# Performance work log

Measured on AMD Instinct MI355X. Metric: run time of the kernel, lower is better.

The kernel has to match this reference:

```python
import jax, jax.numpy as jnp
import numpy as np

N = 10000          # nodes
E = 160000         # random edges (self-loops added in reference, as PyG does)
HEADS = 32
DIMS = [4, 128, 512, 1028]
NEG_SLOPE_ATT = 0.2    # GATv2Conv default negative_slope
NEG_SLOPE_ACT = 0.01   # torch.nn.LeakyReLU default


def setup_inputs() -> dict:
    key = jax.random.key(0)
    ks = jax.random.split(key, 32)
    inp = {}
    inp["x"] = jax.random.normal(ks[0], (N, DIMS[0]), dtype=jnp.float32)
    inp["edge_index"] = jax.random.randint(ks[1], (2, E), 0, N, dtype=jnp.int32)
    k = 2
    for l in range(3):
        fi, fo = DIMS[l], DIMS[l + 1]
        s_in = 1.0 / np.sqrt(fi)
        s_att = 1.0 / np.sqrt(fo)
        inp[f"W{l+1}l"] = (jax.random.normal(ks[k], (fi, HEADS * fo)) * s_in).astype(jnp.float32); k += 1
        inp[f"b{l+1}l"] = jnp.zeros((HEADS * fo,), jnp.float32)
        inp[f"W{l+1}r"] = (jax.random.normal(ks[k], (fi, HEADS * fo)) * s_in).astype(jnp.float32); k += 1
        inp[f"b{l+1}r"] = jnp.zeros((HEADS * fo,), jnp.float32)
        inp[f"att{l+1}"] = (jax.random.normal(ks[k], (HEADS, fo)) * s_att).astype(jnp.float32); k += 1
        inp[f"bias{l+1}"] = jnp.zeros((fo,), jnp.float32)
    return inp


def gatv2_layer(x, src, dst, Wl, bl, Wr, br, att, bias):
    # x: [N, fi]; src/dst: [E'] (self-loops included); att: [H, C]
    H, C = att.shape
    n = x.shape[0]
    xl = (x @ Wl + bl).reshape(n, H, C)  # source transform
    xr = (x @ Wr + br).reshape(n, H, C)  # target transform

    def per_head(args):
        xlh, xrh, ah = args  # [N,C], [N,C], [C]
        s = jax.nn.leaky_relu(xlh[src] + xrh[dst], NEG_SLOPE_ATT)  # [E',C]
        e = s @ ah  # [E'] attention logits
        m = jax.ops.segment_max(e, dst, num_segments=n)
        p = jnp.exp(e - m[dst])
        den = jax.ops.segment_sum(p, dst, num_segments=n)
        alpha = p / den[dst]  # edge-softmax per destination
        return jax.ops.segment_sum(alpha[:, None] * xlh[src], dst, num_segments=n)  # [N,C]

    # iterate heads sequentially to keep peak memory at O(E*C), not O(E*H*C)
    out = jax.lax.map(per_head, (jnp.moveaxis(xl, 1, 0), jnp.moveaxis(xr, 1, 0), att))  # [H,N,C]
    return out.mean(axis=0) + bias  # concat=False -> head mean


def reference(x, edge_index, W1l, b1l, W1r, b1r, att1, bias1,
              W2l, b2l, W2r, b2r, att2, bias2,
              W3l, b3l, W3r, b3r, att3, bias3):
    n = x.shape[0]
    loop = jnp.arange(n, dtype=edge_index.dtype)
    src = jnp.concatenate([edge_index[0], loop])
    dst = jnp.concatenate([edge_index[1], loop])
    h = gatv2_layer(x, src, dst, W1l, b1l, W1r, b1r, att1, bias1)
    h = jax.nn.leaky_relu(h, NEG_SLOPE_ACT)
    h = gatv2_layer(h, src, dst, W2l, b2l, W2r, b2r, att2, bias2)
    h = jax.nn.leaky_relu(h, NEG_SLOPE_ACT)
    h = gatv2_layer(h, src, dst, W3l, b3l, W3r, b3r, att3, bias3)
    return h
```

## Files before the change

kernel.cpp:

```cpp
#include <hip/hip_runtime.h>
#include <cstddef>
#include <cstdint>


#define HEADS 32
#define SLOPE_ATT 0.2f
#define SLOPE_ACT 0.01f

typedef __bf16 bf16_t;
typedef __bf16 bf16x8 __attribute__((ext_vector_type(8)));
typedef float f32x16 __attribute__((ext_vector_type(16)));

#define GLDS16(gp, lp)                                                        \
  __builtin_amdgcn_global_load_lds(                                           \
      (const __attribute__((address_space(1))) void*)(gp),                    \
      (__attribute__((address_space(3))) void*)(lp), 16, 0, 0)


__global__ __launch_bounds__(256) void init_counts_kernel(int* counts, int n) {
  int i = blockIdx.x * 256 + threadIdx.x;
  if (i < n) counts[i] = 1;
}

__global__ __launch_bounds__(256) void count_kernel(const int* __restrict__ dst, int* counts, int E) {
  int e = blockIdx.x * 256 + threadIdx.x;
  if (e < E) atomicAdd(&counts[dst[e]], 1);
}

__global__ __launch_bounds__(1024) void scan_kernel(const int* __restrict__ counts,
                                                    int* __restrict__ row_ptr,
                                                    int* __restrict__ cursor, int n) {
  __shared__ int sums[1024];
  int t = threadIdx.x;
  int per = (n + 1023) >> 10;
  int base = t * per;
  int s = 0;
  for (int i = 0; i < per; i++) { int idx = base + i; if (idx < n) s += counts[idx]; }
  sums[t] = s;
  __syncthreads();
  for (int off = 1; off < 1024; off <<= 1) {
    int v = (t >= off) ? sums[t - off] : 0;
    __syncthreads();
    sums[t] += v;
    __syncthreads();
  }
  int run = (t == 0) ? 0 : sums[t - 1];
  for (int i = 0; i < per; i++) {
    int idx = base + i;
    if (idx < n) { row_ptr[idx] = run; cursor[idx] = run; run += counts[idx]; }
  }
  if (t == 1023) row_ptr[n] = sums[1023];
}

__global__ __launch_bounds__(256) void scatter_edges_kernel(const int* __restrict__ ei, int* cursor,
                                                            int* col_src, int* col_dst, int E) {
  int e = blockIdx.x * 256 + threadIdx.x;
  if (e >= E) return;
  int src = ei[e], dst = ei[E + e];
  int pos = atomicAdd(&cursor[dst], 1);
  col_src[pos] = src;
  col_dst[pos] = dst;
}

__global__ __launch_bounds__(256) void scatter_loops_kernel(int* cursor, int* col_src, int* col_dst, int N) {
  int nid = blockIdx.x * 256 + threadIdx.x;
  if (nid >= N) return;
  int pos = atomicAdd(&cursor[nid], 1);
  col_src[pos] = nid;
  col_dst[pos] = nid;
}


__global__ __launch_bounds__(256) void cvt_pack_kernel(const float* __restrict__ X,
                                                       bf16_t* __restrict__ hi,
                                                       bf16_t* __restrict__ lo,
                                                       int M, int Mpad, int K) {
  int t = blockIdx.x * 256 + threadIdx.x;
  int kchunks = K >> 3;
  int total = Mpad * kchunks;
  if (t >= total) return;
  int kc = t % kchunks;
  int m = t / kchunks;
  int mt = m >> 7, ml = m & 127;
  size_t o = ((size_t)(mt * kchunks + kc)) * 1024 + (size_t)ml * 8;
  float v[8];
  if (m < M) {
    float4 a = *(const float4*)(X + (size_t)m * K + kc * 8);
    float4 b = *(const float4*)(X + (size_t)m * K + kc * 8 + 4);
    v[0] = a.x; v[1] = a.y; v[2] = a.z; v[3] = a.w;
    v[4] = b.x; v[5] = b.y; v[6] = b.z; v[7] = b.w;
  } else {
#pragma unroll
    for (int i = 0; i < 8; i++) v[i] = 0.f;
  }
  union { bf16_t h[8]; float4 f; } uh, ul;
#pragma unroll
  for (int i = 0; i < 8; i++) {
    bf16_t h = (bf16_t)v[i];
    uh.h[i] = h;
    ul.h[i] = (bf16_t)(v[i] - (float)h);
  }
  *(float4*)(hi + o) = uh.f;
  *(float4*)(lo + o) = ul.f;
}


__global__ __launch_bounds__(256) void pack_w_group_kernel(const float* __restrict__ Wl,
                                                           const float* __restrict__ Wr,
                                                           bf16_t* __restrict__ hL, bf16_t* __restrict__ lL,
                                                           bf16_t* __restrict__ hR, bf16_t* __restrict__ lR,
                                                           int K, int C, int Npad, int ldW,
                                                           int h0, int G) {
  int side = blockIdx.y;
  const float* W = side ? Wr : Wl;
  bf16_t* Hi = side ? hR : hL;
  bf16_t* Lo = side ? lR : lL;
  int kchunks = K >> 3;
  int perhead = Npad * kchunks;
  int t = blockIdx.x * 256 + threadIdx.x;
  if (t >= G * perhead) return;
  int g = t / perhead, rem = t % perhead;
  int n = rem % Npad, kc = rem / Npad;
  int nt = n >> 7, nl = n & 127;
  size_t o = (size_t)g * Npad * K + ((size_t)(nt * kchunks + kc)) * 1024 + (size_t)nl * 8;
  int col0 = (h0 + g) * C;
  union { bf16_t hh[8]; float4 f; } uh, ul;
#pragma unroll
  for (int kk = 0; kk < 8; kk++) {
    int k = kc * 8 + kk;
    float v = (n < C) ? W[(size_t)k * ldW + col0 + n] : 0.f;
    bf16_t hv = (bf16_t)v;
    uh.hh[kk] = hv;
    ul.hh[kk] = (bf16_t)(v - (float)hv);
  }
  *(float4*)(Hi + o) = uh.f;
  *(float4*)(Lo + o) = ul.f;
}


__global__ __launch_bounds__(256) void gemm_mfma_v6(const bf16_t* __restrict__ Xh,
                                                    const bf16_t* __restrict__ Xl,
                                                    const bf16_t* __restrict__ BhL,
                                                    const bf16_t* __restrict__ BlL,
                                                    const bf16_t* __restrict__ BhR,
                                                    const bf16_t* __restrict__ BlR,
                                                    size_t bHeadStride,
                                                    const float* __restrict__ bl,
                                                    const float* __restrict__ br,
                                                    float* __restrict__ outL,
                                                    float* __restrict__ outR,
                                                    size_t outHeadStride,
                                                    int M, int K, int C, int h0) {
  int g = blockIdx.z >> 1, side = blockIdx.z & 1;
  const bf16_t* Bh = (side ? BhR : BhL) + (size_t)g * bHeadStride;
  const bf16_t* Bl = (side ? BlR : BlL) + (size_t)g * bHeadStride;
  const float* bias = side ? br : bl;
  float* out = (side ? outR : outL) + (size_t)g * outHeadStride;
  int col0 = (h0 + g) * C;

  __shared__ __align__(16) bf16_t AsH[4 * 128 * 8];
  __shared__ __align__(16) bf16_t AsL[4 * 128 * 8];
  __shared__ __align__(16) bf16_t BsH[4 * 128 * 8];
  __shared__ __align__(16) bf16_t BsL[4 * 128 * 8];

  int tid = threadIdx.x;
  int wave = tid >> 6, lane = tid & 63;
  int l31 = lane & 31, lhalf = lane >> 5;
  int mt = blockIdx.y;
  int ntb = blockIdx.x * 128;
  int m0 = mt * 128;
  int kchunks = K >> 3;

  const bf16_t* Ah = Xh + (size_t)mt * K * 128;
  const bf16_t* Al = Xl + (size_t)mt * K * 128;
  const bf16_t* Bhp = Bh + (size_t)blockIdx.x * kchunks * 1024;
  const bf16_t* Blp = Bl + (size_t)blockIdx.x * kchunks * 1024;

  auto* asH3 = (__attribute__((address_space(3))) bf16_t*)AsH;
  auto* asL3 = (__attribute__((address_space(3))) bf16_t*)AsL;
  auto* bsH3 = (__attribute__((address_space(3))) bf16_t*)BsH;
  auto* bsL3 = (__attribute__((address_space(3))) bf16_t*)BsL;

  f32x16 acc[4];
#pragma unroll
  for (int i = 0; i < 4; i++)
#pragma unroll
    for (int r = 0; r < 16; r++) acc[i][r] = 0.f;

  for (int k0 = 0; k0 < K; k0 += 32) {
    int kc0 = k0 >> 3;
#pragma unroll
    for (int r = 0; r < 2; r++) {
      int idx = tid + 256 * r;
      size_t off = ((size_t)(kc0 + (idx >> 7))) * 1024 + (size_t)(idx & 127) * 8;
      int li = idx * 8;
      GLDS16(Ah + off, asH3 + li);
      GLDS16(Al + off, asL3 + li);
      GLDS16(Bhp + off, bsH3 + li);
      GLDS16(Blp + off, bsL3 + li);
    }
    __syncthreads();

#pragma unroll
    for (int s = 0; s < 2; s++) {
      int c = s * 2 + lhalf;
      int abase = (c * 128 + wave * 32 + l31) * 8;
      bf16x8 ah = *(const bf16x8*)&AsH[abase];
      bf16x8 al = *(const bf16x8*)&AsL[abase];
#pragma unroll
      for (int nt = 0; nt < 4; nt++) {
        int bbase = (c * 128 + nt * 32 + l31) * 8;
        bf16x8 bh = *(const bf16x8*)&BsH[bbase];
        bf16x8 blo = *(const bf16x8*)&BsL[bbase];
        acc[nt] = __builtin_amdgcn_mfma_f32_32x32x16_bf16(ah, bh, acc[nt], 0, 0, 0);
        acc[nt] = __builtin_amdgcn_mfma_f32_32x32x16_bf16(ah, blo, acc[nt], 0, 0, 0);
        acc[nt] = __builtin_amdgcn_mfma_f32_32x32x16_bf16(al, bh, acc[nt], 0, 0, 0);
      }
    }
    __syncthreads();
  }

#pragma unroll
  for (int nt = 0; nt < 4; nt++) {
    int n = ntb + nt * 32 + l31;
    if (n >= C) continue;
    float bv = bias[col0 + n];
#pragma unroll
    for (int r = 0; r < 16; r++) {
      int row = (r & 3) + 8 * (r >> 2) + 4 * lhalf;
      int m = m0 + wave * 32 + row;
      if (m < M) out[(size_t)m * C + n] = acc[nt][r] + bv;
    }
  }
}


#define BM 128
#define BN 128
#define BK 16
#define LDA (BM + 4)
#define LDB (BN + 4)

__global__ __launch_bounds__(256) void gemm128(const float* __restrict__ X,
                                               const float* __restrict__ Wl,
                                               const float* __restrict__ Wr,
                                               const float* __restrict__ bl,
                                               const float* __restrict__ br,
                                               float* __restrict__ outL,
                                               float* __restrict__ outR,
                                               int M, int K, int C, int ldW, int col0) {
  const float* W = blockIdx.z ? Wr : Wl;
  const float* bias = blockIdx.z ? br : bl;
  float* out = blockIdx.z ? outR : outL;

  __shared__ __align__(16) float As[BK][LDA];
  __shared__ __align__(16) float Bs[BK][LDB];

  int t = threadIdx.x;
  int tx = t & 15, ty = t >> 4;
  int m0 = blockIdx.y * BM, n0 = blockIdx.x * BN;

  float acc00[4][4] = {}, acc01[4][4] = {}, acc10[4][4] = {}, acc11[4][4] = {};

  for (int k0 = 0; k0 < K; k0 += BK) {
    {
      int kk = (t & 3) * 4;
#pragma unroll
      for (int p = 0; p < 2; p++) {
        int row = (t >> 2) + p * 64;
        int m = m0 + row;
        float4 v = make_float4(0.f, 0.f, 0.f, 0.f);
        if (m < M && (k0 + kk) < K)
          v = *(const float4*)(X + (size_t)m * K + k0 + kk);
        As[kk + 0][row] = v.x; As[kk + 1][row] = v.y;
        As[kk + 2][row] = v.z; As[kk + 3][row] = v.w;
      }
    }
    {
      int kk = t >> 4;
#pragma unroll
      for (int q = 0; q < 2; q++) {
        int cn = (t & 15) * 4 + q * 64;
        int n = n0 + cn;
        float4 v = make_float4(0.f, 0.f, 0.f, 0.f);
        if ((k0 + kk) < K && n + 3 < C)
          v = *(const float4*)(W + (size_t)(k0 + kk) * ldW + col0 + n);
        *(float4*)&Bs[kk][cn] = v;
      }
    }
    __syncthreads();

    int kmax = min(BK, K - k0);
    for (int kk = 0; kk < kmax; kk++) {
      float4 a0 = *(const float4*)&As[kk][ty * 4];
      float4 a1 = *(const float4*)&As[kk][64 + ty * 4];
      float4 b0 = *(const float4*)&Bs[kk][tx * 4];
      float4 b1 = *(const float4*)&Bs[kk][64 + tx * 4];
      float af0[4] = {a0.x, a0.y, a0.z, a0.w};
      float af1[4] = {a1.x, a1.y, a1.z, a1.w};
      float bf0[4] = {b0.x, b0.y, b0.z, b0.w};
      float bf1[4] = {b1.x, b1.y, b1.z, b1.w};
#pragma unroll
      for (int i = 0; i < 4; i++)
#pragma unroll
        for (int j = 0; j < 4; j++) {
          acc00[i][j] += af0[i] * bf0[j];
          acc01[i][j] += af0[i] * bf1[j];
          acc10[i][j] += af1[i] * bf0[j];
          acc11[i][j] += af1[i] * bf1[j];
        }
    }
    __syncthreads();
  }

#pragma unroll
  for (int ma = 0; ma < 2; ma++) {
#pragma unroll
    for (int i = 0; i < 4; i++) {
      int m = m0 + ma * 64 + ty * 4 + i;
      if (m >= M) continue;
#pragma unroll
      for (int nb = 0; nb < 2; nb++) {
        int n = n0 + nb * 64 + tx * 4;
        float (*blk)[4] = (ma == 0) ? ((nb == 0) ? acc00 : acc01)
                                    : ((nb == 0) ? acc10 : acc11);
        if (n + 3 < C) {
          float4 bv = *(const float4*)(bias + col0 + n);
          float4 o = make_float4(blk[i][0] + bv.x, blk[i][1] + bv.y,
                                 blk[i][2] + bv.z, blk[i][3] + bv.w);
          *(float4*)(out + (size_t)m * C + n) = o;
        }
      }
    }
  }
}


template <int F4PT>
__global__ __launch_bounds__(256) void edge_fused_kernel(const int* __restrict__ row_ptr,
                                                         const int* __restrict__ col_src,
                                                         const float* __restrict__ xl,
                                                         const float* __restrict__ xr,
                                                         int ld4, int coff4,
                                                         const float* __restrict__ att,
                                                         float* __restrict__ acc,
                                                         int C, int head) {
  int node = blockIdx.x;
  int tid = threadIdx.x;
  int wave = tid >> 6, lane = tid & 63;
  int C4 = C >> 2;
  int s = row_ptr[node], t = row_ptr[node + 1];

  __shared__ __align__(16) float4 slab[4][F4PT * 64];
  __shared__ float mred[4], dred[4];

  float4 xr4[F4PT], a4[F4PT], o4[F4PT];
  const float4* xrp = (const float4*)xr + (size_t)node * ld4 + coff4;
  const float4* ap = (const float4*)att;
#pragma unroll
  for (int k = 0; k < F4PT; k++) {
    int c4 = k * 64 + lane;
    bool ok = (c4 < C4);
    xr4[k] = ok ? xrp[c4] : make_float4(0.f, 0.f, 0.f, 0.f);
    a4[k] = ok ? ap[c4] : make_float4(0.f, 0.f, 0.f, 0.f);
    o4[k] = make_float4(0.f, 0.f, 0.f, 0.f);
  }
  float m = -1e30f, den = 0.f;

  for (int j = s + wave; j < t; j += 4) {
    int src = col_src[j];
    const float4* xlp = (const float4*)xl + (size_t)src * ld4 + coff4;
    float4 x4[F4PT];
    float e = 0.f;
#pragma unroll
    for (int k = 0; k < F4PT; k++) {
      int c4 = k * 64 + lane;
      x4[k] = (c4 < C4) ? xlp[c4] : make_float4(0.f, 0.f, 0.f, 0.f);
      float v;
      v = x4[k].x + xr4[k].x; v = fmaxf(v, 0.f) + SLOPE_ATT * fminf(v, 0.f); e += a4[k].x * v;
      v = x4[k].y + xr4[k].y; v = fmaxf(v, 0.f) + SLOPE_ATT * fminf(v, 0.f); e += a4[k].y * v;
      v = x4[k].z + xr4[k].z; v = fmaxf(v, 0.f) + SLOPE_ATT * fminf(v, 0.f); e += a4[k].z * v;
      v = x4[k].w + xr4[k].w; v = fmaxf(v, 0.f) + SLOPE_ATT * fminf(v, 0.f); e += a4[k].w * v;
    }
#pragma unroll
    for (int off = 1; off < 64; off <<= 1) e += __shfl_xor(e, off, 64);

    if (e <= m) {
      float p = expf(e - m);
      den += p;
#pragma unroll
      for (int k = 0; k < F4PT; k++) {
        o4[k].x += p * x4[k].x; o4[k].y += p * x4[k].y;
        o4[k].z += p * x4[k].z; o4[k].w += p * x4[k].w;
      }
    } else {
      float scale = expf(m - e);
      den = den * scale + 1.f;
#pragma unroll
      for (int k = 0; k < F4PT; k++) {
        o4[k].x = o4[k].x * scale + x4[k].x; o4[k].y = o4[k].y * scale + x4[k].y;
        o4[k].z = o4[k].z * scale + x4[k].z; o4[k].w = o4[k].w * scale + x4[k].w;
      }
      m = e;
    }
  }

  if (lane == 0) { mred[wave] = m; dred[wave] = den; }
  __syncthreads();
  float M2 = fmaxf(fmaxf(mred[0], mred[1]), fmaxf(mred[2], mred[3]));
  float dtot = dred[0] * expf(mred[0] - M2) + dred[1] * expf(mred[1] - M2) +
               dred[2] * expf(mred[2] - M2) + dred[3] * expf(mred[3] - M2);
  float f = expf(m - M2);
#pragma unroll
  for (int k = 0; k < F4PT; k++) {
    float4 w4 = make_float4(o4[k].x * f, o4[k].y * f, o4[k].z * f, o4[k].w * f);
    slab[wave][k * 64 + lane] = w4;
  }
  __syncthreads();
  float inv = 1.0f / dtot;
  float4* accp = (float4*)(acc + (size_t)node * C);
  for (int c4 = tid; c4 < C4; c4 += 256) {
    float4 s0 = slab[0][c4], s1 = slab[1][c4], s2 = slab[2][c4], s3 = slab[3][c4];
    float4 val = make_float4(((s0.x + s1.x) + (s2.x + s3.x)) * inv,
                             ((s0.y + s1.y) + (s2.y + s3.y)) * inv,
                             ((s0.z + s1.z) + (s2.z + s3.z)) * inv,
                             ((s0.w + s1.w) + (s2.w + s3.w)) * inv);
    if (head == 0) {
      accp[c4] = val;
    } else {
      float4 prev = accp[c4];
      accp[c4] = make_float4(prev.x + val.x, prev.y + val.y, prev.z + val.z, prev.w + val.w);
    }
  }
}


__global__ __launch_bounds__(256) void finalize_kernel(const float* __restrict__ acc,
                                                       const float* __restrict__ bias,
                                                       float* __restrict__ out,
                                                       int total, int C, int apply_act) {
  int i = blockIdx.x * 256 + threadIdx.x;
  if (i >= total) return;
  int c = i % C;
  float v = acc[i] * (1.0f / 32.0f) + bias[c];
  if (apply_act) v = (v >= 0.f) ? v : SLOPE_ACT * v;
  out[i] = v;
}


static inline size_t align16(size_t x) { return (x + 15) & ~size_t(15); }

extern "C" void kernel_launch(void* const* d_in, const int* in_sizes, int n_in,
                              void* d_out, int out_size, void* d_ws, size_t ws_size,
                              hipStream_t stream) {
  const float* x0 = (const float*)d_in[0];
  const int* ei = (const int*)d_in[1];

  const int N = in_sizes[0] / 4;
  const int E = in_sizes[1] / 2;
  const int ETOT = E + N;
  const int MTILES = (N + 127) / 128;
  const int MPAD = MTILES * 128;

  struct LayerP { const float *Wl, *bl, *Wr, *br, *att, *bias; int fi, fo; };
  LayerP L[3] = {
      {(const float*)d_in[2],  (const float*)d_in[3],  (const float*)d_in[4],
       (const float*)d_in[5],  (const float*)d_in[6],  (const float*)d_in[7],  4, 128},
      {(const float*)d_in[8],  (const float*)d_in[9],  (const float*)d_in[10],
       (const float*)d_in[11], (const float*)d_in[12], (const float*)d_in[13], 128, 512},
      {(const float*)d_in[14], (const float*)d_in[15], (const float*)d_in[16],
       (const float*)d_in[17], (const float*)d_in[18], (const float*)d_in[19], 512, 1028},
  };

  char* w = (char*)d_ws;
  auto alloc = [&](size_t bytes) { char* p = w; w += align16(bytes); return p; };
  int* counts   = (int*)alloc((size_t)N * 4);
  int* row_ptr  = (int*)alloc((size_t)(N + 1) * 4);
  int* cursor   = (int*)alloc((size_t)N * 4);
  int* col_src  = (int*)alloc((size_t)ETOT * 4);
  int* col_dst  = (int*)alloc((size_t)ETOT * 4);
  float* xlh    = (float*)alloc((size_t)N * 2056 * 4);
  float* xrh    = (float*)alloc((size_t)N * 2056 * 4);
  float* h1     = (float*)alloc((size_t)N * 128 * 4);
  float* h2     = (float*)alloc((size_t)N * 512 * 4);
  float* acc12  = (float*)alloc((size_t)N * 512 * 4);
  bf16_t* xph   = (bf16_t*)alloc((size_t)MPAD * 512 * 2);
  bf16_t* xpl   = (bf16_t*)alloc((size_t)MPAD * 512 * 2);
  const size_t WPK3 = (size_t)2 * 1152 * 512;
  bf16_t* w3hL  = (bf16_t*)alloc(WPK3 * 2);
  bf16_t* w3lL  = (bf16_t*)alloc(WPK3 * 2);
  bf16_t* w3hR  = (bf16_t*)alloc(WPK3 * 2);
  bf16_t* w3lR  = (bf16_t*)alloc(WPK3 * 2);
  const size_t WPK2 = (size_t)HEADS * 512 * 128;
  bf16_t* w2hL  = (bf16_t*)alloc(WPK2 * 2);
  bf16_t* w2lL  = (bf16_t*)alloc(WPK2 * 2);
  bf16_t* w2hR  = (bf16_t*)alloc(WPK2 * 2);
  bf16_t* w2lR  = (bf16_t*)alloc(WPK2 * 2);

  init_counts_kernel<<<(N + 255) / 256, 256, 0, stream>>>(counts, N);
  count_kernel<<<(E + 255) / 256, 256, 0, stream>>>(ei + E, counts, E);
  scan_kernel<<<1, 1024, 0, stream>>>(counts, row_ptr, cursor, N);
  scatter_edges_kernel<<<(E + 255) / 256, 256, 0, stream>>>(ei, cursor, col_src, col_dst, E);
  scatter_loops_kernel<<<(N + 255) / 256, 256, 0, stream>>>(cursor, col_src, col_dst, N);

  {
    int C = 128;
    float* acc = acc12;
    for (int g = 0; g < 4; g++) {
      dim3 ggrid(8, MTILES, 2);
      gemm128<<<ggrid, 256, 0, stream>>>(x0, L[0].Wl, L[0].Wr, L[0].bl, L[0].br,
                                         xlh, xrh, N, 4, 1024, HEADS * C, g * 1024);
      for (int hh = 0; hh < 8; hh++) {
        int head = g * 8 + hh;
        edge_fused_kernel<1><<<N, 256, 0, stream>>>(row_ptr, col_src, xlh, xrh,
                                                    256, hh * 32,
                                                    L[0].att + (size_t)head * C, acc, C, head);
      }
    }
    finalize_kernel<<<((size_t)N * C + 255) / 256, 256, 0, stream>>>(acc, L[0].bias, h1,
                                                                     N * C, C, 1);
  }

  {
    int fi = 128, C = 512, ldW = HEADS * C, Npadh = 512, G = 4;
    float* acc = acc12;
    size_t NC = (size_t)N * C;
    int total = MPAD * (fi >> 3);
    cvt_pack_kernel<<<(total + 255) / 256, 256, 0, stream>>>(h1, xph, xpl, N, MPAD, fi);
    int wtotal = HEADS * Npadh * (fi >> 3);
    dim3 wgrid((wtotal + 255) / 256, 2);
    pack_w_group_kernel<<<wgrid, 256, 0, stream>>>(L[1].Wl, L[1].Wr, w2hL, w2lL, w2hR, w2lR,
                                                   fi, C, Npadh, ldW, 0, HEADS);
    size_t hstride = (size_t)Npadh * fi;
    for (int h0 = 0; h0 < HEADS; h0 += G) {
      dim3 ggrid(Npadh / 128, MTILES, 2 * G);
      gemm_mfma_v6<<<ggrid, 256, 0, stream>>>(xph, xpl,
                                              w2hL + h0 * hstride, w2lL + h0 * hstride,
                                              w2hR + h0 * hstride, w2lR + h0 * hstride,
                                              hstride, L[1].bl, L[1].br,
                                              xlh, xrh, NC, N, fi, C, h0);
      for (int g = 0; g < G; g++) {
        int head = h0 + g;
        edge_fused_kernel<2><<<N, 256, 0, stream>>>(row_ptr, col_src,
                                                    xlh + g * NC, xrh + g * NC, C / 4, 0,
                                                    L[1].att + (size_t)head * C, acc, C, head);
      }
    }
    finalize_kernel<<<((size_t)N * C + 255) / 256, 256, 0, stream>>>(acc, L[1].bias, h2,
                                                                     N * C, C, 1);
  }

  {
    int fi = 512, C = 1028, ldW = HEADS * C, Npadh = 1152, G = 2;
    float* acc = (float*)d_out;
    size_t NC = (size_t)N * C;
    int total = MPAD * (fi >> 3);
    cvt_pack_kernel<<<(total + 255) / 256, 256, 0, stream>>>(h2, xph, xpl, N, MPAD, fi);
    size_t hstride = (size_t)Npadh * fi;
    for (int h0 = 0; h0 < HEADS; h0 += G) {
      int wtotal = G * Npadh * (fi >> 3);
      dim3 wgrid((wtotal + 255) / 256, 2);
      pack_w_group_kernel<<<wgrid, 256, 0, stream>>>(L[2].Wl, L[2].Wr, w3hL, w3lL, w3hR, w3lR,
                                                     fi, C, Npadh, ldW, h0, G);
      dim3 ggrid(Npadh / 128, MTILES, 2 * G);
      gemm_mfma_v6<<<ggrid, 256, 0, stream>>>(xph, xpl, w3hL, w3lL, w3hR, w3lR,
                                              hstride, L[2].bl, L[2].br,
                                              xlh, xrh, NC, N, fi, C, h0);
      for (int g = 0; g < G; g++) {
        int head = h0 + g;
        edge_fused_kernel<5><<<N, 256, 0, stream>>>(row_ptr, col_src,
                                                    xlh + g * NC, xrh + g * NC, C / 4, 0,
                                                    L[2].att + (size_t)head * C, acc, C, head);
      }
    }
    finalize_kernel<<<((size_t)N * C + 255) / 256, 256, 0, stream>>>(acc, L[2].bias, (float*)d_out,
                                                                     N * C, C, 0);
  }
}
```

Baseline: 10.30 ms.

## Fuse per-head edge kernels into one multi-head launch and remap GEMM blocks per XCD

The per-head edge softmax/aggregation kernels are merged into one kernel that loops over a group of heads per node. Each head's contribution is accumulated in registers, and the accumulator in global memory is read and written once per group instead of once per head. This also removes many kernel launches. The MFMA GEMM now remaps its linear block id so that consecutive blocks on each XCD cover a rectangle of M-tiles, aiming for better L2 reuse of the A/B tiles. The cost is more registers for the per-group accumulators and extra index arithmetic at the start of each GEMM block.

```diff
diff --git a/kernel.cpp b/kernel.cpp
--- a/kernel.cpp
+++ b/kernel.cpp
@@ -151,7 +151,34 @@
                                                     float* __restrict__ outR,
                                                     size_t outHeadStride,
                                                     int M, int K, int C, int h0) {
-  int g = blockIdx.z >> 1, side = blockIdx.z & 1;
+  int gx = gridDim.x, gy = gridDim.y, gz = gridDim.z;
+  int nwg = gx * gy * gz;
+  int p = blockIdx.x + gx * (blockIdx.y + gy * blockIdx.z);
+  int q = nwg >> 3, r = nwg & 7;
+  int xcd = p & 7, slot = p >> 3;
+  int lid = (xcd < r ? xcd * (q + 1) : r * (q + 1) + (xcd - r) * q) + slot;
+  const int NY = 8;
+  int xzsz = gx * gz;
+  int fullr = gy / NY;
+  int lidf = fullr * NY * xzsz;
+  int rectbase, ny, rem;
+  if (lid < lidf) {
+    int rect = lid / (NY * xzsz);
+    rem = lid - rect * (NY * xzsz);
+    rectbase = rect * NY;
+    ny = NY;
+  } else {
+    rem = lid - lidf;
+    rectbase = fullr * NY;
+    ny = gy - rectbase;
+  }
+  int xz = rem / ny;
+  int yl = rem - xz * ny;
+  int bx = xz % gx;
+  int bz = xz / gx;
+  int by = rectbase + yl;
+
+  int g = bz >> 1, side = bz & 1;
   const bf16_t* Bh = (side ? BhR : BhL) + (size_t)g * bHeadStride;
   const bf16_t* Bl = (side ? BlR : BlL) + (size_t)g * bHeadStride;
   const float* bias = side ? br : bl;
@@ -166,15 +193,15 @@
   int tid = threadIdx.x;
   int wave = tid >> 6, lane = tid & 63;
   int l31 = lane & 31, lhalf = lane >> 5;
-  int mt = blockIdx.y;
-  int ntb = blockIdx.x * 128;
+  int mt = by;
+  int ntb = bx * 128;
   int m0 = mt * 128;
   int kchunks = K >> 3;
 
   const bf16_t* Ah = Xh + (size_t)mt * K * 128;
   const bf16_t* Al = Xl + (size_t)mt * K * 128;
-  const bf16_t* Bhp = Bh + (size_t)blockIdx.x * kchunks * 1024;
-  const bf16_t* Blp = Bl + (size_t)blockIdx.x * kchunks * 1024;
+  const bf16_t* Bhp = Bh + (size_t)bx * kchunks * 1024;
+  const bf16_t* Blp = Bl + (size_t)bx * kchunks * 1024;
 
   auto* asH3 = (__attribute__((address_space(3))) bf16_t*)AsH;
   auto* asL3 = (__attribute__((address_space(3))) bf16_t*)AsL;
@@ -185,13 +212,13 @@
 #pragma unroll
   for (int i = 0; i < 4; i++)
 #pragma unroll
-    for (int r = 0; r < 16; r++) acc[i][r] = 0.f;
+    for (int rr = 0; rr < 16; rr++) acc[i][rr] = 0.f;
 
   for (int k0 = 0; k0 < K; k0 += 32) {
     int kc0 = k0 >> 3;
 #pragma unroll
-    for (int r = 0; r < 2; r++) {
-      int idx = tid + 256 * r;
+    for (int rr = 0; rr < 2; rr++) {
+      int idx = tid + 256 * rr;
       size_t off = ((size_t)(kc0 + (idx >> 7))) * 1024 + (size_t)(idx & 127) * 8;
       int li = idx * 8;
       GLDS16(Ah + off, asH3 + li);
@@ -226,10 +253,10 @@
     if (n >= C) continue;
     float bv = bias[col0 + n];
 #pragma unroll
-    for (int r = 0; r < 16; r++) {
-      int row = (r & 3) + 8 * (r >> 2) + 4 * lhalf;
+    for (int rr = 0; rr < 16; rr++) {
+      int row = (rr & 3) + 8 * (rr >> 2) + 4 * lhalf;
       int m = m0 + wave * 32 + row;
-      if (m < M) out[(size_t)m * C + n] = acc[nt][r] + bv;
+      if (m < M) out[(size_t)m * C + n] = acc[nt][rr] + bv;
     }
   }
 }
@@ -279,8 +306,8 @@
     {
       int kk = t >> 4;
 #pragma unroll
-      for (int q = 0; q < 2; q++) {
-        int cn = (t & 15) * 4 + q * 64;
+      for (int qq = 0; qq < 2; qq++) {
+        int cn = (t & 15) * 4 + qq * 64;
         int n = n0 + cn;
         float4 v = make_float4(0.f, 0.f, 0.f, 0.f);
         if ((k0 + kk) < K && n + 3 < C)
@@ -337,14 +364,15 @@
 
 
 template <int F4PT>
-__global__ __launch_bounds__(256) void edge_fused_kernel(const int* __restrict__ row_ptr,
-                                                         const int* __restrict__ col_src,
-                                                         const float* __restrict__ xl,
-                                                         const float* __restrict__ xr,
-                                                         int ld4, int coff4,
-                                                         const float* __restrict__ att,
-                                                         float* __restrict__ acc,
-                                                         int C, int head) {
+__global__ __launch_bounds__(256) void edge_fused_multi(const int* __restrict__ row_ptr,
+                                                        const int* __restrict__ col_src,
+                                                        const float* __restrict__ xl,
+                                                        const float* __restrict__ xr,
+                                                        int ld4, size_t hstride4,
+                                                        const float* __restrict__ att,
+                                                        float* __restrict__ acc,
+                                                        int C, int head0, int G) {
+  constexpr int ITER = (F4PT * 64 + 255) / 256;
   int node = blockIdx.x;
   int tid = threadIdx.x;
   int wave = tid >> 6, lane = tid & 63;
@@ -354,82 +382,103 @@
   __shared__ __align__(16) float4 slab[4][F4PT * 64];
   __shared__ float mred[4], dred[4];
 
-  float4 xr4[F4PT], a4[F4PT], o4[F4PT];
-  const float4* xrp = (const float4*)xr + (size_t)node * ld4 + coff4;
-  const float4* ap = (const float4*)att;
-#pragma unroll
-  for (int k = 0; k < F4PT; k++) {
-    int c4 = k * 64 + lane;
-    bool ok = (c4 < C4);
-    xr4[k] = ok ? xrp[c4] : make_float4(0.f, 0.f, 0.f, 0.f);
-    a4[k] = ok ? ap[c4] : make_float4(0.f, 0.f, 0.f, 0.f);
-    o4[k] = make_float4(0.f, 0.f, 0.f, 0.f);
-  }
-  float m = -1e30f, den = 0.f;
-
-  for (int j = s + wave; j < t; j += 4) {
-    int src = col_src[j];
-    const float4* xlp = (const float4*)xl + (size_t)src * ld4 + coff4;
-    float4 x4[F4PT];
-    float e = 0.f;
+  float4 vtot[ITER];
+#pragma unroll
+  for (int it = 0; it < ITER; it++) vtot[it] = make_float4(0.f, 0.f, 0.f, 0.f);
+
+  for (int g = 0; g < G; g++) {
+    const float4* xlb = (const float4*)xl + (size_t)g * hstride4;
+    const float4* xrp = (const float4*)xr + (size_t)g * hstride4 + (size_t)node * ld4;
+    const float4* ap = (const float4*)(att + (size_t)g * C);
+
+    float4 xr4[F4PT], a4[F4PT], o4[F4PT];
 #pragma unroll
     for (int k = 0; k < F4PT; k++) {
       int c4 = k * 64 + lane;
-      x4[k] = (c4 < C4) ? xlp[c4] : make_float4(0.f, 0.f, 0.f, 0.f);
-      float v;
-      v = x4[k].x + xr4[k].x; v = fmaxf(v, 0.f) + SLOPE_ATT * fminf(v, 0.f); e += a4[k].x * v;
-      v = x4[k].y + xr4[k].y; v = fmaxf(v, 0.f) + SLOPE_ATT * fminf(v, 0.f); e += a4[k].y * v;
-      v = x4[k].z + xr4[k].z; v = fmaxf(v, 0.f) + SLOPE_ATT * fminf(v, 0.f); e += a4[k].z * v;
-      v = x4[k].w + xr4[k].w; v = fmaxf(v, 0.f) + SLOPE_ATT * fminf(v, 0.f); e += a4[k].w * v;
-    }
-#pragma unroll
-    for (int off = 1; off < 64; off <<= 1) e += __shfl_xor(e, off, 64);
-
-    if (e <= m) {
-      float p = expf(e - m);
-      den += p;
+      bool ok = (c4 < C4);
+      xr4[k] = ok ? xrp[c4] : make_float4(0.f, 0.f, 0.f, 0.f);
+      a4[k] = ok ? ap[c4] : make_float4(0.f, 0.f, 0.f, 0.f);
+      o4[k] = make_float4(0.f, 0.f, 0.f, 0.f);
+    }
+    float m = -1e30f, den = 0.f;
+
+    for (int j = s + wave; j < t; j += 4) {
+      int src = col_src[j];
+      const float4* xlp = xlb + (size_t)src * ld4;
+      float4 x4[F4PT];
+      float e = 0.f;
 #pragma unroll
       for (int k = 0; k < F4PT; k++) {
-        o4[k].x += p * x4[k].x; o4[k].y += p * x4[k].y;
-        o4[k].z += p * x4[k].z; o4[k].w += p * x4[k].w;
-      }
-    } else {
-      float scale = expf(m - e);
-      den = den * scale + 1.f;
-#pragma unroll
-      for (int k = 0; k < F4PT; k++) {
-        o4[k].x = o4[k].x * scale + x4[k].x; o4[k].y = o4[k].y * scale + x4[k].y;
-        o4[k].z = o4[k].z * scale + x4[k].z; o4[k].w = o4[k].w * scale + x4[k].w;
-      }
-      m = e;
-    }
-  }
-
-  if (lane == 0) { mred[wave] = m; dred[wave] = den; }
-  __syncthreads();
-  float M2 = fmaxf(fmaxf(mred[0], mred[1]), fmaxf(mred[2], mred[3]));
-  float dtot = dred[0] * expf(mred[0] - M2) + dred[1] * expf(mred[1] - M2) +
-               dred[2] * expf(mred[2] - M2) + dred[3] * expf(mred[3] - M2);
-  float f = expf(m - M2);
-#pragma unroll
-  for (int k = 0; k < F4PT; k++) {
-    float4 w4 = make_float4(o4[k].x * f, o4[k].y * f, o4[k].z * f, o4[k].w * f);
-    slab[wave][k * 64 + lane] = w4;
-  }
-  __syncthreads();
-  float inv = 1.0f / dtot;
+        int c4 = k * 64 + lane;
+        x4[k] = (c4 < C4) ? xlp[c4] : make_float4(0.f, 0.f, 0.f, 0.f);
+        float v;
+        v = x4[k].x + xr4[k].x; v = fmaxf(v, 0.f) + SLOPE_ATT * fminf(v, 0.f); e += a4[k].x * v;
+        v = x4[k].y + xr4[k].y; v = fmaxf(v, 0.f) + SLOPE_ATT * fminf(v, 0.f); e += a4[k].y * v;
+        v = x4[k].z + xr4[k].z; v = fmaxf(v, 0.f) + SLOPE_ATT * fminf(v, 0.f); e += a4[k].z * v;
+        v = x4[k].w + xr4[k].w; v = fmaxf(v, 0.f) + SLOPE_ATT * fminf(v, 0.f); e += a4[k].w * v;
+      }
+#pragma unroll
+      for (int off = 1; off < 64; off <<= 1) e += __shfl_xor(e, off, 64);
+
+      if (e <= m) {
+        float p = expf(e - m);
+        den += p;
+#pragma unroll
+        for (int k = 0; k < F4PT; k++) {
+          o4[k].x += p * x4[k].x; o4[k].y += p * x4[k].y;
+          o4[k].z += p * x4[k].z; o4[k].w += p * x4[k].w;
+        }
+      } else {
+        float scale = expf(m - e);
+        den = den * scale + 1.f;
+#pragma unroll
+        for (int k = 0; k < F4PT; k++) {
+          o4[k].x = o4[k].x * scale + x4[k].x; o4[k].y = o4[k].y * scale + x4[k].y;
+          o4[k].z = o4[k].z * scale + x4[k].z; o4[k].w = o4[k].w * scale + x4[k].w;
+        }
+        m = e;
+      }
+    }
+
+    if (lane == 0) { mred[wave] = m; dred[wave] = den; }
+    __syncthreads();
+    float M2 = fmaxf(fmaxf(mred[0], mred[1]), fmaxf(mred[2], mred[3]));
+    float dtot = dred[0] * expf(mred[0] - M2) + dred[1] * expf(mred[1] - M2) +
+                 dred[2] * expf(mred[2] - M2) + dred[3] * expf(mred[3] - M2);
+    float f = expf(m - M2);
+#pragma unroll
+    for (int k = 0; k < F4PT; k++) {
+      float4 w4 = make_float4(o4[k].x * f, o4[k].y * f, o4[k].z * f, o4[k].w * f);
+      slab[wave][k * 64 + lane] = w4;
+    }
+    __syncthreads();
+    float inv = 1.0f / dtot;
+#pragma unroll
+    for (int it = 0; it < ITER; it++) {
+      int c4 = tid + it * 256;
+      if (c4 < C4) {
+        float4 s0 = slab[0][c4], s1 = slab[1][c4], s2 = slab[2][c4], s3 = slab[3][c4];
+        vtot[it].x += ((s0.x + s1.x) + (s2.x + s3.x)) * inv;
+        vtot[it].y += ((s0.y + s1.y) + (s2.y + s3.y)) * inv;
+        vtot[it].z += ((s0.z + s1.z) + (s2.z + s3.z)) * inv;
+        vtot[it].w += ((s0.w + s1.w) + (s2.w + s3.w)) * inv;
+      }
+    }
+    __syncthreads();
+  }
+
   float4* accp = (float4*)(acc + (size_t)node * C);
-  for (int c4 = tid; c4 < C4; c4 += 256) {
-    float4 s0 = slab[0][c4], s1 = slab[1][c4], s2 = slab[2][c4], s3 = slab[3][c4];
-    float4 val = make_float4(((s0.x + s1.x) + (s2.x + s3.x)) * inv,
-                             ((s0.y + s1.y) + (s2.y + s3.y)) * inv,
-                             ((s0.z + s1.z) + (s2.z + s3.z)) * inv,
-                             ((s0.w + s1.w) + (s2.w + s3.w)) * inv);
-    if (head == 0) {
-      accp[c4] = val;
-    } else {
-      float4 prev = accp[c4];
-      accp[c4] = make_float4(prev.x + val.x, prev.y + val.y, prev.z + val.z, prev.w + val.w);
+#pragma unroll
+  for (int it = 0; it < ITER; it++) {
+    int c4 = tid + it * 256;
+    if (c4 < C4) {
+      if (head0 == 0) {
+        accp[c4] = vtot[it];
+      } else {
+        float4 prev = accp[c4];
+        accp[c4] = make_float4(prev.x + vtot[it].x, prev.y + vtot[it].y,
+                               prev.z + vtot[it].z, prev.w + vtot[it].w);
+      }
     }
   }
 }
@@ -510,12 +559,10 @@
       dim3 ggrid(8, MTILES, 2);
       gemm128<<<ggrid, 256, 0, stream>>>(x0, L[0].Wl, L[0].Wr, L[0].bl, L[0].br,
                                          xlh, xrh, N, 4, 1024, HEADS * C, g * 1024);
-      for (int hh = 0; hh < 8; hh++) {
-        int head = g * 8 + hh;
-        edge_fused_kernel<1><<<N, 256, 0, stream>>>(row_ptr, col_src, xlh, xrh,
-                                                    256, hh * 32,
-                                                    L[0].att + (size_t)head * C, acc, C, head);
-      }
+      edge_fused_multi<1><<<N, 256, 0, stream>>>(row_ptr, col_src, xlh, xrh,
+                                                 256, (size_t)32,
+                                                 L[0].att + (size_t)(g * 8) * C,
+                                                 acc, C, g * 8, 8);
     }
     finalize_kernel<<<((size_t)N * C + 255) / 256, 256, 0, stream>>>(acc, L[0].bias, h1,
                                                                      N * C, C, 1);
@@ -539,12 +586,10 @@
                                               w2hR + h0 * hstride, w2lR + h0 * hstride,
                                               hstride, L[1].bl, L[1].br,
                                               xlh, xrh, NC, N, fi, C, h0);
-      for (int g = 0; g < G; g++) {
-        int head = h0 + g;
-        edge_fused_kernel<2><<<N, 256, 0, stream>>>(row_ptr, col_src,
-                                                    xlh + g * NC, xrh + g * NC, C / 4, 0,
-                                                    L[1].att + (size_t)head * C, acc, C, head);
-      }
+      edge_fused_multi<2><<<N, 256, 0, stream>>>(row_ptr, col_src, xlh, xrh,
+                                                 C / 4, NC / 4,
+                                                 L[1].att + (size_t)h0 * C,
+                                                 acc, C, h0, G);
     }
     finalize_kernel<<<((size_t)N * C + 255) / 256, 256, 0, stream>>>(acc, L[1].bias, h2,
                                                                      N * C, C, 1);
@@ -566,12 +611,10 @@
       gemm_mfma_v6<<<ggrid, 256, 0, stream>>>(xph, xpl, w3hL, w3lL, w3hR, w3lR,
                                               hstride, L[2].bl, L[2].br,
                                               xlh, xrh, NC, N, fi, C, h0);
-      for (int g = 0; g < G; g++) {
-        int head = h0 + g;
-        edge_fused_kernel<5><<<N, 256, 0, stream>>>(row_ptr, col_src,
-                                                    xlh + g * NC, xrh + g * NC, C / 4, 0,
-                                                    L[2].att + (size_t)head * C, acc, C, head);
-      }
+      edge_fused_multi<5><<<N, 256, 0, stream>>>(row_ptr, col_src, xlh, xrh,
+                                                 C / 4, NC / 4,
+                                                 L[2].att + (size_t)h0 * C,
+                                                 acc, C, h0, G);
     }
     finalize_kernel<<<((size_t)N * C + 255) / 256, 256, 0, stream>>>(acc, L[2].bias, (float*)d_out,
                                                                      N * C, C, 0);
```

Measured after the change: 9.539 ms. -7.4%, faster.
